# Optimization experiments

Measured on AMD Instinct MI355X. Metric: run time of the kernel, lower is better.

## Reference

```python
import jax, jax.numpy as jnp
import numpy as np

B, N_IN, D_IN, N_OUT, D_OUT, ROUTINGS = 512, 1152, 8, 10, 16, 3


def squash(s, axis=-1):
    # scale = |s|^2 / (1 + |s|^2) / (|s| + 1e-8)
    norm = jnp.linalg.norm(s, axis=axis, keepdims=True)
    return (norm ** 2 / (1.0 + norm ** 2) / (norm + 1e-8)) * s


def setup_inputs() -> dict:
    key = jax.random.key(0)
    k1, k2 = jax.random.split(key)
    x = jax.random.normal(k1, (B, N_IN, D_IN), dtype=jnp.float32)
    weight = 0.01 * jax.random.normal(k2, (N_OUT, N_IN, D_OUT, D_IN), dtype=jnp.float32)
    return {"x": x, "weight": weight}


def reference(x, weight):
    # x: [B, N_IN, D_IN]; weight: [N_OUT, N_IN, D_OUT, D_IN]
    # x_hat[b,o,n,:] = weight[o,n] @ x[b,n]  -> [B, N_OUT, N_IN, D_OUT]
    x_hat = jnp.einsum('onij,bnj->boni', weight, x)
    x_hat_det = jax.lax.stop_gradient(x_hat)

    # routing logits b: [B, N_OUT, N_IN]
    b = jnp.zeros(x_hat.shape[:3], dtype=x_hat.dtype)
    outputs = None
    for i in range(ROUTINGS):
        c = jax.nn.softmax(b, axis=1)  # softmax over output capsules
        if i == ROUTINGS - 1:
            outputs = squash(jnp.sum(c[..., None] * x_hat, axis=2))  # [B, N_OUT, D_OUT]
        else:
            outputs = squash(jnp.sum(c[..., None] * x_hat_det, axis=2))
            # agreement: b += <outputs, x_hat_det> over D_OUT
            b = b + jnp.einsum('bod,bond->bon', outputs, x_hat_det)
    return outputs  # [B, N_OUT, D_OUT]
```

## Files before the change

### kernel.cpp

```cpp
#include <hip/hip_runtime.h>
#include <hip/hip_bf16.h>
#include <hip/hip_fp16.h>

#define B_    512
#define NI    1152
#define NO    10
#define BT    16
#define NBT   32
#define NC    24
#define NCH   48
#define RNDS  6
#define RN    8

#define WBUF_US 12288
#define XBUF_US 1024
#define BUF_US  13312

typedef __attribute__((ext_vector_type(8))) short bf16x8;
typedef __attribute__((ext_vector_type(4))) float f32x4;
typedef __attribute__((ext_vector_type(8))) unsigned short u16x8;

#define SPART_H    ((size_t)NC * NBT * NO * 256)
#define OUTSUM_F32 ((size_t)NBT * NO * 256)
#define XB_US      ((size_t)NBT * NC * RNDS * XBUF_US)
#define WB_US      ((size_t)NC * RNDS * WBUF_US)

__device__ inline unsigned short f2bf(float f) {
    __hip_bfloat16 h = __float2bfloat16(f);
    return *reinterpret_cast<unsigned short*>(&h);
}

__device__ inline void gld_lds16(const void* g, void* lds) {
    __builtin_amdgcn_global_load_lds(
        (const __attribute__((address_space(1))) void*)g,
        (__attribute__((address_space(3))) void*)lds, 16, 0, 0);
}

__global__ __launch_bounds__(256) void cvt_xw(
    const float* __restrict__ x, const float* __restrict__ w,
    unsigned short* __restrict__ xb, unsigned short* __restrict__ wb)
{
    const int blk = blockIdx.x;
    if (blk < 2304) {
        const int t   = blk * 256 + threadIdx.x;
        const int m   = t & 127;
        const int img = t >> 7;
        const int nl  = m >> 4, bl = m & 15;
        const int r   = img % RNDS;
        const int bc  = img / RNDS;
        const int nc  = bc % NC, bt = bc / NC;
        const int b   = bt * BT + bl;
        const int n   = nc * NCH + r * RN + nl;
        const float* src = x + ((size_t)b * NI + n) * 8;
        float4 v0 = *reinterpret_cast<const float4*>(src);
        float4 v1 = *reinterpret_cast<const float4*>(src + 4);
        u16x8 u = { f2bf(v0.x), f2bf(v0.y), f2bf(v0.z), f2bf(v0.w),
                    f2bf(v1.x), f2bf(v1.y), f2bf(v1.z), f2bf(v1.w) };
        *reinterpret_cast<u16x8*>(xb + (size_t)t * 8) = u;
    } else {
        const int t    = (blk - 2304) * 256 + threadIdx.x;
        const int lane = t & 63;
        const int gs   = (t >> 6) % 24;
        const int img  = t / 1536;
        const int hi   = lane >> 4, d = lane & 15;
        const int nl   = gs / 3, oq = gs % 3;
        const int r    = img % RNDS, nc = img / RNDS;
        const int o    = oq * 4 + hi;
        const int n    = nc * NCH + r * RN + nl;
        u16x8 u = {0,0,0,0,0,0,0,0};
        if (o < NO) {
            const float* src = w + ((size_t)o * NI + n) * 128 + d * 8;
            float4 v0 = *reinterpret_cast<const float4*>(src);
            float4 v1 = *reinterpret_cast<const float4*>(src + 4);
            u = (u16x8){ f2bf(v0.x), f2bf(v0.y), f2bf(v0.z), f2bf(v0.w),
                         f2bf(v1.x), f2bf(v1.y), f2bf(v1.z), f2bf(v1.w) };
        }
        *reinterpret_cast<u16x8*>(wb + (size_t)t * 8) = u;
    }
}

union LdsU {
    unsigned short stage[2 * BUF_US];
    uint2 red[4][NO * 64];
};

template<bool UNIFORM>
__global__ __launch_bounds__(256, 3) void caps_iter(
    const unsigned short* __restrict__ xb,
    const unsigned short* __restrict__ wb,
    const float* __restrict__ outsum,
    unsigned short* __restrict__ s_part)
{
    __shared__ LdsU lds;

    const int tid = threadIdx.x;
    const int w   = tid >> 6;
    const int l   = tid & 63;
    const int b16 = l & 15;
    const int hi  = l >> 4;
    const int blk = blockIdx.x;
    const int xcd = blk & 7, idx = blk >> 3;
    const int nc  = xcd * 3 + (idx >> 5);
    const int bt  = idx & 31;

    const unsigned short* wsrc = wb + (size_t)nc * (RNDS * WBUF_US);
    const unsigned short* xsrc = xb + ((size_t)bt * NC + nc) * (RNDS * XBUF_US);

    auto stage = [&](int r, int kbuf) {
        const unsigned short* wr = wsrc + (size_t)r * WBUF_US;
        char* dst = (char*)lds.stage + kbuf * (BUF_US * 2);
        #pragma unroll
        for (int k = 0; k < 6; ++k)
            gld_lds16(wr + (k * 256 + tid) * 8, dst + (k * 256 + tid) * 16);
        if (tid < 128)
            gld_lds16(xsrc + (size_t)r * XBUF_US + tid * 8,
                      dst + WBUF_US * 2 + tid * 16);
    };

    f32x4 outf[NO];
    if constexpr (!UNIFORM) {
        #pragma unroll
        for (int o = 0; o < NO; ++o)
            outf[o] = *reinterpret_cast<const f32x4*>(
                outsum + (((size_t)bt * NO + o) * 64 + l) * 4);
    }

    f32x4 sacc[NO];
    #pragma unroll
    for (int o = 0; o < NO; ++o) sacc[o] = (f32x4){0.f, 0.f, 0.f, 0.f};

    stage(0, 0);
    asm volatile("s_waitcnt vmcnt(0)" ::: "memory");
    __syncthreads();

    #pragma unroll 1
    for (int r = 0; r < RNDS; ++r) {
        if (r + 1 < RNDS) stage(r + 1, (r + 1) & 1);

        const int ub = (r & 1) * BUF_US;

        #pragma unroll 1
        for (int i = 0; i < 2; ++i) {
            const int nl = w * 2 + i;
            bf16x8 bv = *reinterpret_cast<const bf16x8*>(
                &lds.stage[ub + WBUF_US + nl * 128 + b16 * 8]);
            bf16x8 bvt[4];
            #pragma unroll
            for (int t = 0; t < 4; ++t)
                bvt[t] = (hi == t) ? bv : (bf16x8){0,0,0,0,0,0,0,0};

            if constexpr (UNIFORM) {
                #pragma unroll
                for (int oq = 0; oq < 3; ++oq) {
                    bf16x8 av = *reinterpret_cast<const bf16x8*>(
                        &lds.stage[ub + (nl * 3 + oq) * 512 + l * 8]);
                    const int tmax = (oq < 2) ? 4 : 2;
                    #pragma unroll
                    for (int t = 0; t < tmax; ++t)
                        sacc[oq * 4 + t] = __builtin_amdgcn_mfma_f32_16x16x32_bf16(
                            av, bvt[t], sacc[oq * 4 + t], 0, 0, 0);
                }
            } else {
                f32x4 xh[NO];
                float lg[NO];
                #pragma unroll
                for (int oq = 0; oq < 3; ++oq) {
                    bf16x8 av = *reinterpret_cast<const bf16x8*>(
                        &lds.stage[ub + (nl * 3 + oq) * 512 + l * 8]);
                    const int tmax = (oq < 2) ? 4 : 2;
                    #pragma unroll
                    for (int t = 0; t < tmax; ++t) {
                        const int o = oq * 4 + t;
                        xh[o] = __builtin_amdgcn_mfma_f32_16x16x32_bf16(
                            av, bvt[t], (f32x4){0.f, 0.f, 0.f, 0.f}, 0, 0, 0);
                        float pp = outf[o][0] * xh[o][0];
                        pp = fmaf(outf[o][1], xh[o][1], pp);
                        pp = fmaf(outf[o][2], xh[o][2], pp);
                        pp = fmaf(outf[o][3], xh[o][3], pp);
                        pp += __shfl_xor(pp, 16, 64);
                        pp += __shfl_xor(pp, 32, 64);
                        lg[o] = pp;
                    }
                }
                float sum = 0.f;
                #pragma unroll
                for (int o = 0; o < NO; ++o) { lg[o] = __expf(lg[o]); sum += lg[o]; }
                const float rs = __builtin_amdgcn_rcpf(sum);
                #pragma unroll
                for (int o = 0; o < NO; ++o) {
                    const float cc = lg[o] * rs;
                    sacc[o][0] = fmaf(cc, xh[o][0], sacc[o][0]);
                    sacc[o][1] = fmaf(cc, xh[o][1], sacc[o][1]);
                    sacc[o][2] = fmaf(cc, xh[o][2], sacc[o][2]);
                    sacc[o][3] = fmaf(cc, xh[o][3], sacc[o][3]);
                }
            }
        }

        asm volatile("s_waitcnt vmcnt(0)" ::: "memory");
        __syncthreads();
    }

    const float sc = UNIFORM ? 0.1f : 1.0f;
    #pragma unroll
    for (int o = 0; o < NO; ++o) {
        __half2 h01 = __floats2half2_rn(sacc[o][0] * sc, sacc[o][1] * sc);
        __half2 h23 = __floats2half2_rn(sacc[o][2] * sc, sacc[o][3] * sc);
        lds.red[w][o * 64 + l] =
            make_uint2(*reinterpret_cast<unsigned int*>(&h01),
                       *reinterpret_cast<unsigned int*>(&h23));
    }
    __syncthreads();
    unsigned short* base = s_part + ((size_t)nc * NBT + bt) * 2560;
    for (int g = tid; g < NO * 64; g += 256) {
        uint2 a0 = lds.red[0][g], a1 = lds.red[1][g],
              a2 = lds.red[2][g], a3 = lds.red[3][g];
        auto h2f2 = [](unsigned int u) {
            __half2 h = *reinterpret_cast<__half2*>(&u);
            return __half22float2(h);
        };
        float2 lo = h2f2(a0.x), l1 = h2f2(a1.x), l2 = h2f2(a2.x), l3 = h2f2(a3.x);
        float2 ho = h2f2(a0.y), h1 = h2f2(a1.y), h2 = h2f2(a2.y), h3 = h2f2(a3.y);
        float2 sl = { (lo.x + l1.x) + (l2.x + l3.x), (lo.y + l1.y) + (l2.y + l3.y) };
        float2 sh = { (ho.x + h1.x) + (h2.x + h3.x), (ho.y + h1.y) + (h2.y + h3.y) };
        __half2 p01 = __floats2half2_rn(sl.x, sl.y);
        __half2 p23 = __floats2half2_rn(sh.x, sh.y);
        *reinterpret_cast<uint2*>(base + (size_t)g * 4) =
            make_uint2(*reinterpret_cast<unsigned int*>(&p01),
                       *reinterpret_cast<unsigned int*>(&p23));
    }
}

template<int MODE>
__global__ __launch_bounds__(256) void caps_squash(
    const unsigned short* __restrict__ s_part,
    float* __restrict__ outsum,
    float* __restrict__ dout)
{
    __shared__ float sq[256];
    const int bo = blockIdx.x;
    const int t  = threadIdx.x;

    float s = 0.f;
    #pragma unroll 4
    for (int nc = 0; nc < NC; ++nc) {
        __half h = *reinterpret_cast<const __half*>(
            s_part + ((size_t)nc * NBT * NO + bo) * 256 + t);
        s += __half2float(h);
    }

    float n2 = s * s;
    n2 += __shfl_xor(n2, 1, 64);
    n2 += __shfl_xor(n2, 2, 64);
    sq[t] = n2;
    __syncthreads();
    const int base = t & 63;
    n2 = (sq[base] + sq[64 + base]) + (sq[128 + base] + sq[192 + base]);

    const float norm  = sqrtf(n2);
    const float scale = n2 / ((1.f + n2) * (norm + 1e-8f));
    const float v = scale * s;

    if constexpr (MODE == 0) {
        outsum[(size_t)bo * 256 + t] = v;
    } else if constexpr (MODE == 1) {
        outsum[(size_t)bo * 256 + t] += v;
    } else {
        const int bt = bo / NO, o = bo - bt * NO;
        const int b16 = (t >> 2) & 15, hi = t >> 6, q = t & 3;
        dout[((size_t)(bt * BT + b16) * NO + o) * 16 + hi * 4 + q] = v;
    }
}

extern "C" void kernel_launch(void* const* d_in, const int* in_sizes, int n_in,
                              void* d_out, int out_size, void* d_ws, size_t ws_size,
                              hipStream_t stream) {
    const float* x = (const float*)d_in[0];
    const float* w = (const float*)d_in[1];
    float* out = (float*)d_out;

    unsigned short* s_part = (unsigned short*)d_ws;
    float*          outsum = (float*)(s_part + SPART_H);
    unsigned short* xb     = (unsigned short*)(outsum + OUTSUM_F32);
    unsigned short* wb     = xb + XB_US;

    cvt_xw<<<dim3(3168), dim3(256), 0, stream>>>(x, w, xb, wb);

    dim3 gI(NBT * NC), bI(256);
    dim3 gS(NBT * NO), bS(256);

    caps_iter<true ><<<gI, bI, 0, stream>>>(xb, wb, nullptr, s_part);
    caps_squash<0><<<gS, bS, 0, stream>>>(s_part, outsum, nullptr);
    caps_iter<false><<<gI, bI, 0, stream>>>(xb, wb, outsum, s_part);
    caps_squash<1><<<gS, bS, 0, stream>>>(s_part, outsum, nullptr);
    caps_iter<false><<<gI, bI, 0, stream>>>(xb, wb, outsum, s_part);
    caps_squash<2><<<gS, bS, 0, stream>>>(s_part, nullptr, out);
}
```

Measured before the change: 77.59 us.

## Fuse bf16 conversion into first routing pass and drop LDS staging

Removes the separate fp32-to-bf16 conversion kernel and folds it into the first uniform routing pass. That pass now converts x and weight in registers, computes directly from the fp32 inputs with a dense K=32 MFMA packing, and writes the bf16 copies for later passes. The later routing kernels read bf16 operands straight from global memory into registers instead of double-buffering through LDS with global_load_lds. This saves one launch and an extra pass over memory, but the later passes now rely on cache hits rather than explicit LDS prefetch, and the first pass reads weights uncoalesced.

After: 68.27 us. 12.0% less time.

```diff
diff --git a/kernel.cpp b/kernel.cpp
--- a/kernel.cpp
+++ b/kernel.cpp
@@ -12,209 +12,43 @@
 #define RNDS  6
 #define RN    8
 
-#define WBUF_US 12288
-#define XBUF_US 1024
-#define BUF_US  13312
-
 typedef __attribute__((ext_vector_type(8))) short bf16x8;
 typedef __attribute__((ext_vector_type(4))) float f32x4;
 typedef __attribute__((ext_vector_type(8))) unsigned short u16x8;
 
 #define SPART_H    ((size_t)NC * NBT * NO * 256)
 #define OUTSUM_F32 ((size_t)NBT * NO * 256)
-#define XB_US      ((size_t)NBT * NC * RNDS * XBUF_US)
-#define WB_US      ((size_t)NC * RNDS * WBUF_US)
+#define XB_US      ((size_t)NBT * NC * RNDS * 1024)
+#define WB_US      ((size_t)NC * RNDS * 12288)
 
 __device__ inline unsigned short f2bf(float f) {
     __hip_bfloat16 h = __float2bfloat16(f);
     return *reinterpret_cast<unsigned short*>(&h);
 }
 
-__device__ inline void gld_lds16(const void* g, void* lds) {
-    __builtin_amdgcn_global_load_lds(
-        (const __attribute__((address_space(1))) void*)g,
-        (__attribute__((address_space(3))) void*)lds, 16, 0, 0);
-}
-
-__global__ __launch_bounds__(256) void cvt_xw(
-    const float* __restrict__ x, const float* __restrict__ w,
-    unsigned short* __restrict__ xb, unsigned short* __restrict__ wb)
-{
-    const int blk = blockIdx.x;
-    if (blk < 2304) {
-        const int t   = blk * 256 + threadIdx.x;
-        const int m   = t & 127;
-        const int img = t >> 7;
-        const int nl  = m >> 4, bl = m & 15;
-        const int r   = img % RNDS;
-        const int bc  = img / RNDS;
-        const int nc  = bc % NC, bt = bc / NC;
-        const int b   = bt * BT + bl;
-        const int n   = nc * NCH + r * RN + nl;
-        const float* src = x + ((size_t)b * NI + n) * 8;
-        float4 v0 = *reinterpret_cast<const float4*>(src);
-        float4 v1 = *reinterpret_cast<const float4*>(src + 4);
-        u16x8 u = { f2bf(v0.x), f2bf(v0.y), f2bf(v0.z), f2bf(v0.w),
-                    f2bf(v1.x), f2bf(v1.y), f2bf(v1.z), f2bf(v1.w) };
-        *reinterpret_cast<u16x8*>(xb + (size_t)t * 8) = u;
-    } else {
-        const int t    = (blk - 2304) * 256 + threadIdx.x;
-        const int lane = t & 63;
-        const int gs   = (t >> 6) % 24;
-        const int img  = t / 1536;
-        const int hi   = lane >> 4, d = lane & 15;
-        const int nl   = gs / 3, oq = gs % 3;
-        const int r    = img % RNDS, nc = img / RNDS;
-        const int o    = oq * 4 + hi;
-        const int n    = nc * NCH + r * RN + nl;
-        u16x8 u = {0,0,0,0,0,0,0,0};
-        if (o < NO) {
-            const float* src = w + ((size_t)o * NI + n) * 128 + d * 8;
-            float4 v0 = *reinterpret_cast<const float4*>(src);
-            float4 v1 = *reinterpret_cast<const float4*>(src + 4);
-            u = (u16x8){ f2bf(v0.x), f2bf(v0.y), f2bf(v0.z), f2bf(v0.w),
-                         f2bf(v1.x), f2bf(v1.y), f2bf(v1.z), f2bf(v1.w) };
-        }
-        *reinterpret_cast<u16x8*>(wb + (size_t)t * 8) = u;
-    }
-}
-
-union LdsU {
-    unsigned short stage[2 * BUF_US];
-    uint2 red[4][NO * 64];
-};
-
-template<bool UNIFORM>
-__global__ __launch_bounds__(256, 3) void caps_iter(
-    const unsigned short* __restrict__ xb,
-    const unsigned short* __restrict__ wb,
-    const float* __restrict__ outsum,
-    unsigned short* __restrict__ s_part)
-{
-    __shared__ LdsU lds;
-
-    const int tid = threadIdx.x;
-    const int w   = tid >> 6;
-    const int l   = tid & 63;
-    const int b16 = l & 15;
-    const int hi  = l >> 4;
-    const int blk = blockIdx.x;
-    const int xcd = blk & 7, idx = blk >> 3;
-    const int nc  = xcd * 3 + (idx >> 5);
-    const int bt  = idx & 31;
-
-    const unsigned short* wsrc = wb + (size_t)nc * (RNDS * WBUF_US);
-    const unsigned short* xsrc = xb + ((size_t)bt * NC + nc) * (RNDS * XBUF_US);
-
-    auto stage = [&](int r, int kbuf) {
-        const unsigned short* wr = wsrc + (size_t)r * WBUF_US;
-        char* dst = (char*)lds.stage + kbuf * (BUF_US * 2);
-        #pragma unroll
-        for (int k = 0; k < 6; ++k)
-            gld_lds16(wr + (k * 256 + tid) * 8, dst + (k * 256 + tid) * 16);
-        if (tid < 128)
-            gld_lds16(xsrc + (size_t)r * XBUF_US + tid * 8,
-                      dst + WBUF_US * 2 + tid * 16);
-    };
-
-    f32x4 outf[NO];
-    if constexpr (!UNIFORM) {
-        #pragma unroll
-        for (int o = 0; o < NO; ++o)
-            outf[o] = *reinterpret_cast<const f32x4*>(
-                outsum + (((size_t)bt * NO + o) * 64 + l) * 4);
-    }
-
-    f32x4 sacc[NO];
-    #pragma unroll
-    for (int o = 0; o < NO; ++o) sacc[o] = (f32x4){0.f, 0.f, 0.f, 0.f};
-
-    stage(0, 0);
-    asm volatile("s_waitcnt vmcnt(0)" ::: "memory");
-    __syncthreads();
-
-    #pragma unroll 1
-    for (int r = 0; r < RNDS; ++r) {
-        if (r + 1 < RNDS) stage(r + 1, (r + 1) & 1);
-
-        const int ub = (r & 1) * BUF_US;
-
-        #pragma unroll 1
-        for (int i = 0; i < 2; ++i) {
-            const int nl = w * 2 + i;
-            bf16x8 bv = *reinterpret_cast<const bf16x8*>(
-                &lds.stage[ub + WBUF_US + nl * 128 + b16 * 8]);
-            bf16x8 bvt[4];
-            #pragma unroll
-            for (int t = 0; t < 4; ++t)
-                bvt[t] = (hi == t) ? bv : (bf16x8){0,0,0,0,0,0,0,0};
-
-            if constexpr (UNIFORM) {
-                #pragma unroll
-                for (int oq = 0; oq < 3; ++oq) {
-                    bf16x8 av = *reinterpret_cast<const bf16x8*>(
-                        &lds.stage[ub + (nl * 3 + oq) * 512 + l * 8]);
-                    const int tmax = (oq < 2) ? 4 : 2;
-                    #pragma unroll
-                    for (int t = 0; t < tmax; ++t)
-                        sacc[oq * 4 + t] = __builtin_amdgcn_mfma_f32_16x16x32_bf16(
-                            av, bvt[t], sacc[oq * 4 + t], 0, 0, 0);
-                }
-            } else {
-                f32x4 xh[NO];
-                float lg[NO];
-                #pragma unroll
-                for (int oq = 0; oq < 3; ++oq) {
-                    bf16x8 av = *reinterpret_cast<const bf16x8*>(
-                        &lds.stage[ub + (nl * 3 + oq) * 512 + l * 8]);
-                    const int tmax = (oq < 2) ? 4 : 2;
-                    #pragma unroll
-                    for (int t = 0; t < tmax; ++t) {
-                        const int o = oq * 4 + t;
-                        xh[o] = __builtin_amdgcn_mfma_f32_16x16x32_bf16(
-                            av, bvt[t], (f32x4){0.f, 0.f, 0.f, 0.f}, 0, 0, 0);
-                        float pp = outf[o][0] * xh[o][0];
-                        pp = fmaf(outf[o][1], xh[o][1], pp);
-                        pp = fmaf(outf[o][2], xh[o][2], pp);
-                        pp = fmaf(outf[o][3], xh[o][3], pp);
-                        pp += __shfl_xor(pp, 16, 64);
-                        pp += __shfl_xor(pp, 32, 64);
-                        lg[o] = pp;
-                    }
-                }
-                float sum = 0.f;
-                #pragma unroll
-                for (int o = 0; o < NO; ++o) { lg[o] = __expf(lg[o]); sum += lg[o]; }
-                const float rs = __builtin_amdgcn_rcpf(sum);
-                #pragma unroll
-                for (int o = 0; o < NO; ++o) {
-                    const float cc = lg[o] * rs;
-                    sacc[o][0] = fmaf(cc, xh[o][0], sacc[o][0]);
-                    sacc[o][1] = fmaf(cc, xh[o][1], sacc[o][1]);
-                    sacc[o][2] = fmaf(cc, xh[o][2], sacc[o][2]);
-                    sacc[o][3] = fmaf(cc, xh[o][3], sacc[o][3]);
-                }
-            }
-        }
-
-        asm volatile("s_waitcnt vmcnt(0)" ::: "memory");
-        __syncthreads();
-    }
-
-    const float sc = UNIFORM ? 0.1f : 1.0f;
+__device__ __forceinline__ bf16x8 load_cvt8(const float* src) {
+    f32x4 v0 = *reinterpret_cast<const f32x4*>(src);
+    f32x4 v1 = *reinterpret_cast<const f32x4*>(src + 4);
+    u16x8 u = { f2bf(v0[0]), f2bf(v0[1]), f2bf(v0[2]), f2bf(v0[3]),
+                f2bf(v1[0]), f2bf(v1[1]), f2bf(v1[2]), f2bf(v1[3]) };
+    return *reinterpret_cast<bf16x8*>(&u);
+}
+
+__device__ __forceinline__ void iter_epilogue(
+    uint2 (*red)[NO * 64], const f32x4* sacc, float sc,
+    int w, int l, int tid, unsigned short* base)
+{
     #pragma unroll
     for (int o = 0; o < NO; ++o) {
         __half2 h01 = __floats2half2_rn(sacc[o][0] * sc, sacc[o][1] * sc);
         __half2 h23 = __floats2half2_rn(sacc[o][2] * sc, sacc[o][3] * sc);
-        lds.red[w][o * 64 + l] =
+        red[w][o * 64 + l] =
             make_uint2(*reinterpret_cast<unsigned int*>(&h01),
                        *reinterpret_cast<unsigned int*>(&h23));
     }
     __syncthreads();
-    unsigned short* base = s_part + ((size_t)nc * NBT + bt) * 2560;
     for (int g = tid; g < NO * 64; g += 256) {
-        uint2 a0 = lds.red[0][g], a1 = lds.red[1][g],
-              a2 = lds.red[2][g], a3 = lds.red[3][g];
+        uint2 a0 = red[0][g], a1 = red[1][g], a2 = red[2][g], a3 = red[3][g];
         auto h2f2 = [](unsigned int u) {
             __half2 h = *reinterpret_cast<__half2*>(&u);
             return __half22float2(h);
@@ -231,6 +65,164 @@
     }
 }
 
+__global__ __launch_bounds__(256) void caps_f0(
+    const float* __restrict__ x, const float* __restrict__ w,
+    unsigned short* __restrict__ xb, unsigned short* __restrict__ wb,
+    unsigned short* __restrict__ s_part)
+{
+    __shared__ uint2 red[4][NO * 64];
+
+    const int tid = threadIdx.x;
+    const int wv  = tid >> 6;
+    const int l   = tid & 63;
+    const int b16 = l & 15;
+    const int hi  = l >> 4;
+    const int blk = blockIdx.x;
+    const int xcd = blk & 7, idx = blk >> 3;
+    const int nc  = xcd * 3 + (idx >> 5);
+    const int bt  = idx & 31;
+
+    #pragma unroll
+    for (int k = 0; k < 3; ++k) {
+        const int gid = k * 256 + tid;
+        const int r   = gid >> 7, m = gid & 127;
+        const int nl  = m >> 4, bl = m & 15;
+        const int b   = bt * BT + bl;
+        const int n   = nc * NCH + r * RN + nl;
+        const size_t img = (size_t)(bt * NC + nc) * RNDS + r;
+        bf16x8 u = load_cvt8(x + ((size_t)b * NI + n) * 8);
+        *reinterpret_cast<bf16x8*>(xb + (img * 128 + m) * 8) = u;
+    }
+
+    #pragma unroll
+    for (int k = 0; k < 2; ++k) {
+        const int loc = k * 256 + tid;
+        if (loc < 288) {
+            const int t    = blk * 288 + loc;
+            const int lane = t & 63;
+            const int gs   = (t >> 6) % 24;
+            const int img  = t / 1536;
+            const int h2   = lane >> 4, d = lane & 15;
+            const int nl   = gs / 3, oq = gs % 3;
+            const int r    = img % RNDS, ncw = img / RNDS;
+            const int o    = oq * 4 + h2;
+            const int n    = ncw * NCH + r * RN + nl;
+            bf16x8 u = (bf16x8){0,0,0,0,0,0,0,0};
+            if (o < NO)
+                u = load_cvt8(w + ((size_t)o * NI + n) * 128 + d * 8);
+            *reinterpret_cast<bf16x8*>(wb + (size_t)t * 8) = u;
+        }
+    }
+
+    f32x4 sacc[NO];
+    #pragma unroll
+    for (int o = 0; o < NO; ++o) sacc[o] = (f32x4){0.f, 0.f, 0.f, 0.f};
+
+    const int bg = bt * BT + b16;
+    #pragma unroll 1
+    for (int g = 0; g < 3; ++g) {
+        const int n_lane = nc * NCH + wv * 12 + g * 4 + hi;
+        bf16x8 bv4 = load_cvt8(x + ((size_t)bg * NI + n_lane) * 8);
+        #pragma unroll
+        for (int o = 0; o < NO; ++o) {
+            bf16x8 av4 = load_cvt8(w + ((size_t)o * NI + n_lane) * 128 + b16 * 8);
+            sacc[o] = __builtin_amdgcn_mfma_f32_16x16x32_bf16(
+                av4, bv4, sacc[o], 0, 0, 0);
+        }
+    }
+
+    iter_epilogue(red, sacc, 0.1f, wv, l, tid,
+                  s_part + ((size_t)nc * NBT + bt) * 2560);
+}
+
+__global__ __launch_bounds__(256, 3) void caps_itr(
+    const unsigned short* __restrict__ xb,
+    const unsigned short* __restrict__ wb,
+    const float* __restrict__ outsum,
+    unsigned short* __restrict__ s_part)
+{
+    __shared__ uint2 red[4][NO * 64];
+
+    const int tid = threadIdx.x;
+    const int wv  = tid >> 6;
+    const int l   = tid & 63;
+    const int b16 = l & 15;
+    const int hi  = l >> 4;
+    const int blk = blockIdx.x;
+    const int xcd = blk & 7, idx = blk >> 3;
+    const int nc  = xcd * 3 + (idx >> 5);
+    const int bt  = idx & 31;
+
+    f32x4 outf[NO];
+    #pragma unroll
+    for (int o = 0; o < NO; ++o)
+        outf[o] = *reinterpret_cast<const f32x4*>(
+            outsum + (((size_t)bt * NO + o) * 64 + l) * 4);
+
+    f32x4 sacc[NO];
+    #pragma unroll
+    for (int o = 0; o < NO; ++o) sacc[o] = (f32x4){0.f, 0.f, 0.f, 0.f};
+
+    const unsigned short* xbase = xb + (size_t)(bt * NC + nc) * (RNDS * 1024);
+    const unsigned short* wbase = wb + (size_t)nc * (RNDS * 12288);
+
+    #pragma unroll 1
+    for (int r = 0; r < RNDS; ++r) {
+        const unsigned short* xr = xbase + (size_t)r * 1024;
+        const unsigned short* wr = wbase + (size_t)r * 12288;
+        #pragma unroll 1
+        for (int i = 0; i < 2; ++i) {
+            const int nl = wv * 2 + i;
+            bf16x8 bv = *reinterpret_cast<const bf16x8*>(
+                xr + nl * 128 + b16 * 8);
+            bf16x8 avv[3];
+            #pragma unroll
+            for (int oq = 0; oq < 3; ++oq)
+                avv[oq] = *reinterpret_cast<const bf16x8*>(
+                    wr + (nl * 3 + oq) * 512 + l * 8);
+            bf16x8 bvt[4];
+            #pragma unroll
+            for (int t = 0; t < 4; ++t)
+                bvt[t] = (hi == t) ? bv : (bf16x8){0,0,0,0,0,0,0,0};
+
+            f32x4 xh[NO];
+            float lg[NO];
+            #pragma unroll
+            for (int oq = 0; oq < 3; ++oq) {
+                const int tmax = (oq < 2) ? 4 : 2;
+                #pragma unroll
+                for (int t = 0; t < tmax; ++t) {
+                    const int o = oq * 4 + t;
+                    xh[o] = __builtin_amdgcn_mfma_f32_16x16x32_bf16(
+                        avv[oq], bvt[t], (f32x4){0.f, 0.f, 0.f, 0.f}, 0, 0, 0);
+                    float pp = outf[o][0] * xh[o][0];
+                    pp = fmaf(outf[o][1], xh[o][1], pp);
+                    pp = fmaf(outf[o][2], xh[o][2], pp);
+                    pp = fmaf(outf[o][3], xh[o][3], pp);
+                    pp += __shfl_xor(pp, 16, 64);
+                    pp += __shfl_xor(pp, 32, 64);
+                    lg[o] = pp;
+                }
+            }
+            float sum = 0.f;
+            #pragma unroll
+            for (int o = 0; o < NO; ++o) { lg[o] = __expf(lg[o]); sum += lg[o]; }
+            const float rs = __builtin_amdgcn_rcpf(sum);
+            #pragma unroll
+            for (int o = 0; o < NO; ++o) {
+                const float cc = lg[o] * rs;
+                sacc[o][0] = fmaf(cc, xh[o][0], sacc[o][0]);
+                sacc[o][1] = fmaf(cc, xh[o][1], sacc[o][1]);
+                sacc[o][2] = fmaf(cc, xh[o][2], sacc[o][2]);
+                sacc[o][3] = fmaf(cc, xh[o][3], sacc[o][3]);
+            }
+        }
+    }
+
+    iter_epilogue(red, sacc, 1.0f, wv, l, tid,
+                  s_part + ((size_t)nc * NBT + bt) * 2560);
+}
+
 template<int MODE>
 __global__ __launch_bounds__(256) void caps_squash(
     const unsigned short* __restrict__ s_part,
@@ -284,15 +276,13 @@
     unsigned short* xb     = (unsigned short*)(outsum + OUTSUM_F32);
     unsigned short* wb     = xb + XB_US;
 
-    cvt_xw<<<dim3(3168), dim3(256), 0, stream>>>(x, w, xb, wb);
-
     dim3 gI(NBT * NC), bI(256);
     dim3 gS(NBT * NO), bS(256);
 
-    caps_iter<true ><<<gI, bI, 0, stream>>>(xb, wb, nullptr, s_part);
+    caps_f0<<<gI, bI, 0, stream>>>(x, w, xb, wb, s_part);
     caps_squash<0><<<gS, bS, 0, stream>>>(s_part, outsum, nullptr);
-    caps_iter<false><<<gI, bI, 0, stream>>>(xb, wb, outsum, s_part);
+    caps_itr<<<gI, bI, 0, stream>>>(xb, wb, outsum, s_part);
     caps_squash<1><<<gS, bS, 0, stream>>>(s_part, outsum, nullptr);
-    caps_iter<false><<<gI, bI, 0, stream>>>(xb, wb, outsum, s_part);
+    caps_itr<<<gI, bI, 0, stream>>>(xb, wb, outsum, s_part);
     caps_squash<2><<<gS, bS, 0, stream>>>(s_part, nullptr, out);
 }
```
